# Kernel optimization log

Measured on AMD Instinct MI355X. Metric: run time of the kernel, lower is better.

## Reference

```python
import jax, jax.numpy as jnp
import numpy as np

N, E = 100000, 500000
IN_CH, OUT_CH, MSG_DIM, TIME_DIM, HEADS = 128, 128, 128, 128, 2
C = OUT_CH // HEADS  # per-head channels
EDGE_DIM = MSG_DIM + TIME_DIM


def setup_inputs() -> dict:
    key = jax.random.key(0)
    ks = jax.random.split(key, 16)
    inp = {
        "x": jax.random.normal(ks[0], (N, IN_CH), jnp.float32),
        "last_update": jax.random.uniform(ks[1], (N,), jnp.float32) * 1000.0,
        "t": jax.random.uniform(ks[2], (E,), jnp.float32) * 1000.0,
        "msg": jax.random.normal(ks[3], (E, MSG_DIM), jnp.float32),
        "edge_index": jax.random.randint(ks[4], (2, E), 0, N, jnp.int64),
        # TimeEncoder: Linear(1, TIME_DIM) then cos
        "time_w": jax.random.normal(ks[5], (TIME_DIM,), jnp.float32) / jnp.sqrt(1.0),
        "time_b": jax.random.normal(ks[6], (TIME_DIM,), jnp.float32) * 0.02,
        # TransformerConv linears (stored [in, out] for x @ W)
        "Wq": jax.random.normal(ks[7], (IN_CH, HEADS * C), jnp.float32) / np.sqrt(IN_CH),
        "bq": jnp.zeros((HEADS * C,), jnp.float32),
        "Wk": jax.random.normal(ks[8], (IN_CH, HEADS * C), jnp.float32) / np.sqrt(IN_CH),
        "bk": jnp.zeros((HEADS * C,), jnp.float32),
        "Wv": jax.random.normal(ks[9], (IN_CH, HEADS * C), jnp.float32) / np.sqrt(IN_CH),
        "bv": jnp.zeros((HEADS * C,), jnp.float32),
        "We": jax.random.normal(ks[10], (EDGE_DIM, HEADS * C), jnp.float32) / np.sqrt(EDGE_DIM),  # lin_edge, no bias
        "Wskip": jax.random.normal(ks[11], (IN_CH, HEADS * C), jnp.float32) / np.sqrt(IN_CH),
        "bskip": jnp.zeros((HEADS * C,), jnp.float32),
    }
    return inp


def reference(x, last_update, t, msg, edge_index, time_w, time_b,
              Wq, bq, Wk, bk, Wv, bv, We, Wskip, bskip):
    src = edge_index[0]
    dst = edge_index[1]

    # relative time encoding: cos(Linear(1 -> TIME_DIM))
    rel_t = t - last_update[src]                              # [E]
    rel_t_enc = jnp.cos(rel_t[:, None] * time_w[None, :] + time_b[None, :])  # [E, T]
    edge_attr = jnp.concatenate([rel_t_enc, msg], axis=-1)    # [E, EDGE_DIM]

    # project nodes, then gather per-edge (query at dst, key/value at src)
    q = (x @ Wq + bq).reshape(N, HEADS, C)[dst]               # [E, H, C]
    k = (x @ Wk + bk).reshape(N, HEADS, C)[src]
    v = (x @ Wv + bv).reshape(N, HEADS, C)[src]
    e = (edge_attr @ We).reshape(E, HEADS, C)                 # [E, H, C]

    k = k + e
    alpha = jnp.sum(q * k, axis=-1) / jnp.sqrt(jnp.float32(C))  # [E, H]

    # segment softmax over edges sharing the same destination node
    m = jax.ops.segment_max(alpha, dst, num_segments=N)       # [N, H]
    alpha = jnp.exp(alpha - m[dst])
    s = jax.ops.segment_sum(alpha, dst, num_segments=N)       # [N, H]
    alpha = alpha / (s[dst] + 1e-16)

    # weighted value (value also receives edge projection), scatter-add to dst
    out_e = (v + e) * alpha[..., None]                        # [E, H, C]
    out = jax.ops.segment_sum(out_e, dst, num_segments=N)     # [N, H, C]
    out = out.reshape(N, HEADS * C)

    # root/skip connection
    out = out + x @ Wskip + bskip
    return out
```

## Files before the change

### kernel.cpp

```cpp
#include <hip/hip_runtime.h>
#include <hip/hip_bf16.h>

#define NN 100000
#define EE 500000

typedef __attribute__((ext_vector_type(8))) short short8v;
typedef __attribute__((ext_vector_type(4))) float f32x4;

__device__ __forceinline__ short f2bf(float f) {
  unsigned u = __builtin_bit_cast(unsigned, f);
  u += 0x7fffu + ((u >> 16) & 1u);
  return (short)(u >> 16);
}

__device__ __forceinline__ void barlds() {
  asm volatile("s_waitcnt lgkmcnt(0)" ::: "memory");
  __builtin_amdgcn_s_barrier();
  asm volatile("" ::: "memory");
}

__global__ __launch_bounds__(256) void k_prep(
    const float* __restrict__ Wq, const float* __restrict__ Wk,
    const float* __restrict__ Wv, const float* __restrict__ Wsk,
    const float* __restrict__ We,
    short* __restrict__ Btfrag, short* __restrict__ Wefrag)
{
  int idx = blockIdx.x * 256 + threadIdx.x;
  if (idx < 65536) {
    int b = idx & 7, lane = (idx >> 3) & 63, kt = (idx >> 9) & 3, tn = (idx >> 11) & 7, cb = idx >> 14;
    int k = kt * 32 + (lane >> 4) * 8 + b;
    int c = tn * 16 + (lane & 15);
    const float* W = cb == 0 ? Wq : cb == 1 ? Wk : cb == 2 ? Wv : Wsk;
    Btfrag[idx] = f2bf(W[k * 128 + c]);
  } else if (idx < 98304) {
    int i2 = idx - 65536;
    int b = i2 & 7, lane = (i2 >> 3) & 63, kt = (i2 >> 9) & 7, strip = i2 >> 12;
    int k = kt * 32 + (lane >> 4) * 8 + b;
    int c = strip * 16 + (lane & 15);
    Wefrag[i2] = f2bf(We[k * 128 + c]);
  }
}

__global__ __launch_bounds__(256) void k_xcast(const float* __restrict__ x,
                                               unsigned short* __restrict__ xb)
{
  size_t base = ((size_t)blockIdx.x * 256 + threadIdx.x) * 8;
  f32x4 a = *(const f32x4*)(x + base);
  f32x4 b = *(const f32x4*)(x + base + 4);
  short8v w;
  #pragma unroll
  for (int j = 0; j < 4; ++j) { w[j] = f2bf(a[j]); w[4 + j] = f2bf(b[j]); }
  *(short8v*)(xb + base) = w;
}

__global__ __launch_bounds__(256) void k_zero(int* __restrict__ p, int n)
{
  int i = blockIdx.x * 256 + threadIdx.x;
  if (i < n) p[i] = 0;
}

__global__ __launch_bounds__(256) void k_hist(const int* __restrict__ ei, int* __restrict__ cnt)
{
  int e = blockIdx.x * 256 + threadIdx.x;
  if (e < EE) atomicAdd(&cnt[ei[EE + e]], 1);
}

__global__ __launch_bounds__(256) void k_scan_a(const int* __restrict__ cnt,
    int* __restrict__ offtmp, int* __restrict__ bsum)
{
  __shared__ int sc[256];
  int t = threadIdx.x;
  int i = blockIdx.x * 256 + t;
  int v = (i < NN) ? cnt[i] : 0;
  sc[t] = v;
  __syncthreads();
  for (int d = 1; d < 256; d <<= 1) {
    int add = (t >= d) ? sc[t - d] : 0;
    __syncthreads();
    sc[t] += add;
    __syncthreads();
  }
  if (i < NN) offtmp[i] = sc[t] - v;
  if (t == 255) bsum[blockIdx.x] = sc[255];
}

__global__ __launch_bounds__(512) void k_scan_b(const int* __restrict__ bsum,
                                                int* __restrict__ bbase)
{
  __shared__ int sc[512];
  int t = threadIdx.x;
  int v = (t < 391) ? bsum[t] : 0;
  sc[t] = v;
  __syncthreads();
  for (int d = 1; d < 512; d <<= 1) {
    int add = (t >= d) ? sc[t - d] : 0;
    __syncthreads();
    sc[t] += add;
    __syncthreads();
  }
  bbase[t] = sc[t] - v;
}

__global__ __launch_bounds__(256) void k_scatter(const int* __restrict__ ei,
    const float* __restrict__ tt, const float* __restrict__ lu,
    const int* __restrict__ offtmp, const int* __restrict__ bbase,
    int* __restrict__ cur, int4* __restrict__ emeta)
{
  int e = blockIdx.x * 256 + threadIdx.x;
  if (e < EE) {
    int d = ei[EE + e];
    int pos = offtmp[d] + bbase[d >> 8] + atomicAdd(&cur[d], 1);
    int sv = ei[e];
    int4 m;
    m.x = e; m.y = sv; m.z = d;
    m.w = __float_as_int(tt[e] - lu[sv]);
    emeta[pos] = m;
  }
}

template<int USE_MP>
__global__ __launch_bounds__(512) void k_main(
    const unsigned short* __restrict__ xb, const float* __restrict__ msg,
    const unsigned short* __restrict__ msgb,
    const float* __restrict__ tw, const float* __restrict__ tb,
    const short* __restrict__ Btfrag, const short* __restrict__ Wefrag,
    const float* __restrict__ bq, const float* __restrict__ bk,
    const float* __restrict__ bv, const float* __restrict__ bsk,
    const int* __restrict__ offtmp, const int* __restrict__ bbase,
    const int4* __restrict__ emeta, float* __restrict__ out)
{
  __shared__ short R[24576];
  __shared__ short QL[64 * 128];
  __shared__ float sdenL[128];
  __shared__ int dslot[64];

  short* const XS = R;
  short* const EAT = R + 8192;
  short* const KL = R;
  short* const VT = R + 8192;
  short* const PLm = R + 16384;
  short* const PLm2 = R + 20480;

  const int tid = threadIdx.x;
  const int nb0 = blockIdx.x * 64;
  const int wid = tid >> 6, lane = tid & 63;
  const int g = lane >> 4, lr = lane & 15, l7 = lr & 7;
  const int el = tid >> 3, p = tid & 7;
  const int er7 = el & 7;
  const int psw = p ^ er7;
  const int cme = wid * 16 + lr;
  const int cmeh = cme >> 3, cml = cme & 7;

  const float bqc = bq[cme], bkc = bk[cme], bvc = bv[cme], bskc = bsk[cme];
  const short8v ONEB = {16256,16256,16256,16256,16256,16256,16256,16256};

  {
    int node = nb0 + el;
    short8v a = {0,0,0,0,0,0,0,0}, b = a;
    if (node < NN) {
      const unsigned short* xp = xb + (size_t)node * 128 + p * 8;
      a = *(const short8v*)xp;
      b = *(const short8v*)(xp + 64);
    }
    *(short8v*)&XS[el * 128 + psw * 8] = a;
    *(short8v*)&XS[el * 128 + psw * 8 + 64] = b;
  }
  barlds();
  f32x4 skp[4];
  {
    f32x4 qacc[4];
    #pragma unroll
    for (int eg = 0; eg < 4; ++eg) {
      qacc[eg] = (f32x4){0.f, 0.f, 0.f, 0.f};
      skp[eg] = qacc[eg];
    }
    #pragma unroll
    for (int kt = 0; kt < 4; ++kt) {
      short8v bqf = *(const short8v*)(Btfrag + (size_t)(((0 + wid) * 4 + kt) * 64 + lane) * 8);
      short8v bsf = *(const short8v*)(Btfrag + (size_t)(((24 + wid) * 4 + kt) * 64 + lane) * 8);
      const int sw = (((kt << 2) | g) ^ l7) << 3;
      #pragma unroll
      for (int eg = 0; eg < 4; ++eg) {
        const short8v a = *(const short8v*)&XS[(eg * 16 + lr) * 128 + sw];
        qacc[eg] = __builtin_amdgcn_mfma_f32_16x16x32_bf16(a, bqf, qacc[eg], 0, 0, 0);
        skp[eg] = __builtin_amdgcn_mfma_f32_16x16x32_bf16(a, bsf, skp[eg], 0, 0, 0);
      }
    }
    #pragma unroll
    for (int eg = 0; eg < 4; ++eg)
      #pragma unroll
      for (int rg = 0; rg < 4; ++rg) {
        int row = eg * 16 + g * 4 + rg;
        QL[row * 128 + ((cmeh ^ (row & 7)) << 3) + cml] = f2bf(qacc[eg][rg] + bqc);
      }
  }

  const int beg = offtmp[nb0] + bbase[nb0 >> 8];
  const int end = (nb0 + 64 < NN) ? (offtmp[nb0 + 64] + bbase[(nb0 + 64) >> 8]) : EE;

  f32x4 acc[4], sdacc;
  #pragma unroll
  for (int rtt = 0; rtt < 4; ++rtt) acc[rtt] = (f32x4){0.f, 0.f, 0.f, 0.f};
  sdacc = (f32x4){0.f, 0.f, 0.f, 0.f};

  int pdst = 0; float prelt = 0.f; bool pval = false;
  short8v px0 = {0,0,0,0,0,0,0,0}, px1 = px0, pmb0 = px0, pmb1 = px0;
  {
    int i = beg + el;
    pval = i < end;
    if (pval) {
      int4 m = emeta[i];
      pdst = m.z; prelt = __int_as_float(m.w);
      const unsigned short* xp = xb + (size_t)m.y * 128 + p * 8;
      px0 = *(const short8v*)xp;
      px1 = *(const short8v*)(xp + 64);
      if constexpr (USE_MP) {
        const unsigned short* mp = msgb + (size_t)m.x * 128 + p * 8;
        pmb0 = *(const short8v*)mp;
        pmb1 = *(const short8v*)(mp + 64);
      } else {
        const float* mp = msg + (size_t)m.x * 128 + p * 8;
        f32x4 m0 = *(const f32x4*)mp,        m1 = *(const f32x4*)(mp + 4);
        f32x4 m2 = *(const f32x4*)(mp + 64), m3 = *(const f32x4*)(mp + 68);
        #pragma unroll
        for (int j = 0; j < 4; ++j) {
          pmb0[j] = f2bf(m0[j]); pmb0[4 + j] = f2bf(m1[j]);
          pmb1[j] = f2bf(m2[j]); pmb1[4 + j] = f2bf(m3[j]);
        }
      }
    }
  }
  barlds();

  for (int t0 = beg; t0 < end; t0 += 64) {
    if (p == 0) dslot[el] = pval ? (pdst - nb0) : -1;
    *(short8v*)&XS[el * 128 + psw * 8] = px0;
    *(short8v*)&XS[el * 128 + psw * 8 + 64] = px1;
    *(short8v*)&EAT[el * 256 + 128 + psw * 8] = pmb0;
    *(short8v*)&EAT[el * 256 + 128 + psw * 8 + 64] = pmb1;
    {
      f32x4 w0 = *(const f32x4*)(tw + p * 8),      w1 = *(const f32x4*)(tw + p * 8 + 4);
      f32x4 b0 = *(const f32x4*)(tb + p * 8),      b1 = *(const f32x4*)(tb + p * 8 + 4);
      f32x4 w2 = *(const f32x4*)(tw + p * 8 + 64), w3 = *(const f32x4*)(tw + p * 8 + 68);
      f32x4 b2 = *(const f32x4*)(tb + p * 8 + 64), b3 = *(const f32x4*)(tb + p * 8 + 68);
      short8v ta, tb2;
      #pragma unroll
      for (int j = 0; j < 4; ++j) {
        ta[j]      = f2bf(__cosf(fmaf(prelt, w0[j], b0[j])));
        ta[4 + j]  = f2bf(__cosf(fmaf(prelt, w1[j], b1[j])));
        tb2[j]     = f2bf(__cosf(fmaf(prelt, w2[j], b2[j])));
        tb2[4 + j] = f2bf(__cosf(fmaf(prelt, w3[j], b3[j])));
      }
      *(short8v*)&EAT[el * 256 + psw * 8] = ta;
      *(short8v*)&EAT[el * 256 + psw * 8 + 64] = tb2;
    }
    barlds();

    {
      int i = t0 + 64 + el;
      pval = i < end;
      if (pval) {
        int4 m = emeta[i];
        pdst = m.z; prelt = __int_as_float(m.w);
        const unsigned short* xp = xb + (size_t)m.y * 128 + p * 8;
        px0 = *(const short8v*)xp;
        px1 = *(const short8v*)(xp + 64);
        if constexpr (USE_MP) {
          const unsigned short* mp = msgb + (size_t)m.x * 128 + p * 8;
          pmb0 = *(const short8v*)mp;
          pmb1 = *(const short8v*)(mp + 64);
        } else {
          const float* mp = msg + (size_t)m.x * 128 + p * 8;
          f32x4 m0 = *(const f32x4*)mp,        m1 = *(const f32x4*)(mp + 4);
          f32x4 m2 = *(const f32x4*)(mp + 64), m3 = *(const f32x4*)(mp + 68);
          #pragma unroll
          for (int j = 0; j < 4; ++j) {
            pmb0[j] = f2bf(m0[j]); pmb0[4 + j] = f2bf(m1[j]);
            pmb1[j] = f2bf(m2[j]); pmb1[4 + j] = f2bf(m3[j]);
          }
        }
      }
    }

    f32x4 ae[4];
    ae[0] = (f32x4){0.f, 0.f, 0.f, 0.f}; ae[1] = ae[0]; ae[2] = ae[0]; ae[3] = ae[0];
    #pragma unroll
    for (int kt = 0; kt < 8; ++kt) {
      short8v wef = *(const short8v*)(Wefrag + (size_t)((wid * 8 + kt) * 64 + lane) * 8);
      const int sw = (((kt << 2) | g) ^ l7) << 3;
      #pragma unroll
      for (int eg = 0; eg < 4; ++eg) {
        const short8v a = *(const short8v*)&EAT[(eg * 16 + lr) * 256 + sw];
        ae[eg] = __builtin_amdgcn_mfma_f32_16x16x32_bf16(a, wef, ae[eg], 0, 0, 0);
      }
    }
    f32x4 ak[4], av[4];
    ak[0] = (f32x4){0.f, 0.f, 0.f, 0.f}; ak[1] = ak[0]; ak[2] = ak[0]; ak[3] = ak[0];
    av[0] = ak[0]; av[1] = ak[0]; av[2] = ak[0]; av[3] = ak[0];
    #pragma unroll
    for (int kt = 0; kt < 4; ++kt) {
      short8v wkf = *(const short8v*)(Btfrag + (size_t)(((8 + wid) * 4 + kt) * 64 + lane) * 8);
      short8v wvf = *(const short8v*)(Btfrag + (size_t)(((16 + wid) * 4 + kt) * 64 + lane) * 8);
      const int sw = (((kt << 2) | g) ^ l7) << 3;
      #pragma unroll
      for (int eg = 0; eg < 4; ++eg) {
        const short8v a = *(const short8v*)&XS[(eg * 16 + lr) * 128 + sw];
        ak[eg] = __builtin_amdgcn_mfma_f32_16x16x32_bf16(a, wkf, ak[eg], 0, 0, 0);
        av[eg] = __builtin_amdgcn_mfma_f32_16x16x32_bf16(a, wvf, av[eg], 0, 0, 0);
      }
    }
    barlds();

    #pragma unroll
    for (int eg = 0; eg < 4; ++eg)
      #pragma unroll
      for (int rg = 0; rg < 4; ++rg) {
        int e = eg * 16 + g * 4 + rg;
        float kh = ak[eg][rg] + bkc + ae[eg][rg];
        float vh = av[eg][rg] + bvc + ae[eg][rg];
        KL[e * 128 + ((cmeh ^ (e & 7)) << 3) + cml] = f2bf(kh);
        VT[cme * 64 + ((((e >> 3) ^ cml)) << 3) + (e & 7)] = f2bf(vh);
      }
    barlds();

    {
      const int rt = wid >> 1, ct0 = (wid & 1) * 2;
      short8v qa[4];
      #pragma unroll
      for (int kt = 0; kt < 4; ++kt)
        qa[kt] = *(const short8v*)&QL[(rt * 16 + lr) * 128 + ((((kt << 2) | g) ^ l7) << 3)];
      #pragma unroll
      for (int c2 = 0; c2 < 2; ++c2) {
        const int ct = ct0 + c2;
        f32x4 s0 = (f32x4){0.f, 0.f, 0.f, 0.f};
        f32x4 s1 = (f32x4){0.f, 0.f, 0.f, 0.f};
        #pragma unroll
        for (int kt = 0; kt < 4; ++kt) {
          const short8v kbf = *(const short8v*)&KL[(ct * 16 + lr) * 128 + ((((kt << 2) | g) ^ l7) << 3)];
          if (kt < 2) s0 = __builtin_amdgcn_mfma_f32_16x16x32_bf16(qa[kt], kbf, s0, 0, 0, 0);
          else        s1 = __builtin_amdgcn_mfma_f32_16x16x32_bf16(qa[kt], kbf, s1, 0, 0, 0);
        }
        const int col = ct * 16 + lr;
        const int dsc = dslot[col];
        #pragma unroll
        for (int rg = 0; rg < 4; ++rg) {
          int row = rt * 16 + g * 4 + rg;
          bool hit = (dsc == row);
          float pv0 = hit ? __expf(s0[rg] * 0.125f) : 0.f;
          float pv1 = hit ? __expf(s1[rg] * 0.125f) : 0.f;
          int off = row * 64 + ((((col >> 3) ^ (row & 7))) << 3) + (col & 7);
          PLm[off] = f2bf(pv0);
          PLm2[off] = f2bf(pv1);
        }
      }
    }
    barlds();

    {
      const short* PH = (wid < 4) ? PLm : PLm2;
      const int rt4 = wid & 3;
      const short8v vb0 = *(const short8v*)&VT[cme * 64 + ((g ^ cml) << 3)];
      const short8v vb1 = *(const short8v*)&VT[cme * 64 + (((4 | g) ^ cml) << 3)];
      #pragma unroll
      for (int rtt = 0; rtt < 4; ++rtt) {
        const short8v pa0 = *(const short8v*)&PH[(rtt * 16 + lr) * 64 + ((g ^ l7) << 3)];
        const short8v pa1 = *(const short8v*)&PH[(rtt * 16 + lr) * 64 + (((4 | g) ^ l7) << 3)];
        acc[rtt] = __builtin_amdgcn_mfma_f32_16x16x32_bf16(pa0, vb0, acc[rtt], 0, 0, 0);
        acc[rtt] = __builtin_amdgcn_mfma_f32_16x16x32_bf16(pa1, vb1, acc[rtt], 0, 0, 0);
        if (rt4 == rtt) {
          sdacc = __builtin_amdgcn_mfma_f32_16x16x32_bf16(pa0, ONEB, sdacc, 0, 0, 0);
          sdacc = __builtin_amdgcn_mfma_f32_16x16x32_bf16(pa1, ONEB, sdacc, 0, 0, 0);
        }
      }
    }
    barlds();
  }

  if (lr == 0) {
    #pragma unroll
    for (int rg = 0; rg < 4; ++rg)
      sdenL[(wid >> 2) * 64 + (wid & 3) * 16 + g * 4 + rg] = sdacc[rg];
  }
  barlds();
  #pragma unroll
  for (int rtt = 0; rtt < 4; ++rtt)
    #pragma unroll
    for (int rg = 0; rg < 4; ++rg) {
      int row = rtt * 16 + g * 4 + rg;
      int node = nb0 + row;
      if (node < NN) {
        float den = sdenL[(wid >> 2) * 64 + row] + 1e-16f;
        out[(size_t)node * 128 + cme] = skp[rtt][rg] + bskc + acc[rtt][rg] / den;
      }
    }
}

extern "C" void kernel_launch(void* const* d_in, const int* in_sizes, int n_in,
                              void* d_out, int out_size, void* d_ws, size_t ws_size,
                              hipStream_t stream) {
  const float* x    = (const float*)d_in[0];
  const float* lu   = (const float*)d_in[1];
  const float* tt   = (const float*)d_in[2];
  const float* msg  = (const float*)d_in[3];
  const int*   ei   = (const int*)d_in[4];
  const float* timew = (const float*)d_in[5];
  const float* timeb = (const float*)d_in[6];
  const float* Wq   = (const float*)d_in[7];
  const float* bq   = (const float*)d_in[8];
  const float* Wk   = (const float*)d_in[9];
  const float* bk   = (const float*)d_in[10];
  const float* Wv   = (const float*)d_in[11];
  const float* bv   = (const float*)d_in[12];
  const float* We   = (const float*)d_in[13];
  const float* Wsk  = (const float*)d_in[14];
  const float* bsk  = (const float*)d_in[15];
  float* out = (float*)d_out;

  char* wsp = (char*)d_ws;
  unsigned short* xbw  = (unsigned short*)wsp;
  short* Btfrag = (short*)(wsp + 51200000);
  short* Wefrag = (short*)(wsp + 51331072);
  int* cnt      = (int*)(wsp + 51404800);
  int* cur      = (int*)(wsp + 51804800);
  int* offtmp   = (int*)(wsp + 52204800);
  int* bsum     = (int*)(wsp + 52605184);
  int* bbase    = (int*)(wsp + 52607232);
  int4* emeta   = (int4*)(wsp + 54609280);
  unsigned short* msgb = (unsigned short*)(wsp + 62609280);
  const int use_mp = (ws_size >= (size_t)190609280) ? 1 : 0;

  k_zero<<<782, 256, 0, stream>>>(cnt, 200000);
  k_prep<<<384, 256, 0, stream>>>(Wq, Wk, Wv, Wsk, We, Btfrag, Wefrag);
  k_xcast<<<6250, 256, 0, stream>>>(x, xbw);
  if (use_mp) k_xcast<<<31250, 256, 0, stream>>>(msg, msgb);
  k_hist<<<1954, 256, 0, stream>>>(ei, cnt);
  k_scan_a<<<391, 256, 0, stream>>>(cnt, offtmp, bsum);
  k_scan_b<<<1, 512, 0, stream>>>(bsum, bbase);
  k_scatter<<<1954, 256, 0, stream>>>(ei, tt, lu, offtmp, bbase, cur, emeta);
  if (use_mp) {
    k_main<1><<<1563, 512, 0, stream>>>(xbw, msg, msgb, timew, timeb,
                                        Btfrag, Wefrag, bq, bk, bv, bsk,
                                        offtmp, bbase, emeta, out);
  } else {
    k_main<0><<<1563, 512, 0, stream>>>(xbw, msg, msgb, timew, timeb,
                                        Btfrag, Wefrag, bq, bk, bv, bsk,
                                        offtmp, bbase, emeta, out);
  }
}
```

Measured before the change: 418.4 us.

## Unalias LDS buffers to drop barriers, pad strides, and drop msg bf16 precast

Gives the main kernel separate padded LDS buffers for x, msg, time encoding, Q, K, V and P instead of one aliased region. With no aliasing, the barrier between the K/V projection and the K/V stores, and the barrier at the end of each edge-tile iteration, can both be removed. The separate msg pre-cast kernel and its bf16 buffer are also removed, so the main kernel always reads fp32 msg and converts it inline. This trades a large increase in LDS per block, which likely cuts blocks per CU, and more global bytes read in the main kernel, for fewer barriers and one less full pass over msg.

```diff
diff --git a/kernel.cpp b/kernel.cpp
--- a/kernel.cpp
+++ b/kernel.cpp
@@ -118,10 +118,8 @@
   }
 }
 
-template<int USE_MP>
 __global__ __launch_bounds__(512) void k_main(
     const unsigned short* __restrict__ xb, const float* __restrict__ msg,
-    const unsigned short* __restrict__ msgb,
     const float* __restrict__ tw, const float* __restrict__ tb,
     const short* __restrict__ Btfrag, const short* __restrict__ Wefrag,
     const float* __restrict__ bq, const float* __restrict__ bk,
@@ -129,17 +127,16 @@
     const int* __restrict__ offtmp, const int* __restrict__ bbase,
     const int4* __restrict__ emeta, float* __restrict__ out)
 {
-  __shared__ short R[24576];
-  __shared__ short QL[64 * 128];
+  __shared__ short XS[64 * 136];
+  __shared__ short MS[64 * 136];
+  __shared__ short TEs[64 * 136];
+  __shared__ short QL[64 * 136];
+  __shared__ short KL[64 * 136];
+  __shared__ short VT[128 * 72];
+  __shared__ short PLm[64 * 72];
+  __shared__ short PLm2[64 * 72];
   __shared__ float sdenL[128];
   __shared__ int dslot[64];
-
-  short* const XS = R;
-  short* const EAT = R + 8192;
-  short* const KL = R;
-  short* const VT = R + 8192;
-  short* const PLm = R + 16384;
-  short* const PLm2 = R + 20480;
 
   const int tid = threadIdx.x;
   const int nb0 = blockIdx.x * 64;
@@ -162,8 +159,8 @@
       a = *(const short8v*)xp;
       b = *(const short8v*)(xp + 64);
     }
-    *(short8v*)&XS[el * 128 + psw * 8] = a;
-    *(short8v*)&XS[el * 128 + psw * 8 + 64] = b;
+    *(short8v*)&XS[el * 136 + psw * 8] = a;
+    *(short8v*)&XS[el * 136 + psw * 8 + 64] = b;
   }
   barlds();
   f32x4 skp[4];
@@ -181,7 +178,7 @@
       const int sw = (((kt << 2) | g) ^ l7) << 3;
       #pragma unroll
       for (int eg = 0; eg < 4; ++eg) {
-        const short8v a = *(const short8v*)&XS[(eg * 16 + lr) * 128 + sw];
+        const short8v a = *(const short8v*)&XS[(eg * 16 + lr) * 136 + sw];
         qacc[eg] = __builtin_amdgcn_mfma_f32_16x16x32_bf16(a, bqf, qacc[eg], 0, 0, 0);
         skp[eg] = __builtin_amdgcn_mfma_f32_16x16x32_bf16(a, bsf, skp[eg], 0, 0, 0);
       }
@@ -191,7 +188,7 @@
       #pragma unroll
       for (int rg = 0; rg < 4; ++rg) {
         int row = eg * 16 + g * 4 + rg;
-        QL[row * 128 + ((cmeh ^ (row & 7)) << 3) + cml] = f2bf(qacc[eg][rg] + bqc);
+        QL[row * 136 + ((cmeh ^ (row & 7)) << 3) + cml] = f2bf(qacc[eg][rg] + bqc);
       }
   }
 
@@ -214,19 +211,13 @@
       const unsigned short* xp = xb + (size_t)m.y * 128 + p * 8;
       px0 = *(const short8v*)xp;
       px1 = *(const short8v*)(xp + 64);
-      if constexpr (USE_MP) {
-        const unsigned short* mp = msgb + (size_t)m.x * 128 + p * 8;
-        pmb0 = *(const short8v*)mp;
-        pmb1 = *(const short8v*)(mp + 64);
-      } else {
-        const float* mp = msg + (size_t)m.x * 128 + p * 8;
-        f32x4 m0 = *(const f32x4*)mp,        m1 = *(const f32x4*)(mp + 4);
-        f32x4 m2 = *(const f32x4*)(mp + 64), m3 = *(const f32x4*)(mp + 68);
-        #pragma unroll
-        for (int j = 0; j < 4; ++j) {
-          pmb0[j] = f2bf(m0[j]); pmb0[4 + j] = f2bf(m1[j]);
-          pmb1[j] = f2bf(m2[j]); pmb1[4 + j] = f2bf(m3[j]);
-        }
+      const float* mp = msg + (size_t)m.x * 128 + p * 8;
+      f32x4 m0 = *(const f32x4*)mp,        m1 = *(const f32x4*)(mp + 4);
+      f32x4 m2 = *(const f32x4*)(mp + 64), m3 = *(const f32x4*)(mp + 68);
+      #pragma unroll
+      for (int j = 0; j < 4; ++j) {
+        pmb0[j] = f2bf(m0[j]); pmb0[4 + j] = f2bf(m1[j]);
+        pmb1[j] = f2bf(m2[j]); pmb1[4 + j] = f2bf(m3[j]);
       }
     }
   }
@@ -234,10 +225,10 @@
 
   for (int t0 = beg; t0 < end; t0 += 64) {
     if (p == 0) dslot[el] = pval ? (pdst - nb0) : -1;
-    *(short8v*)&XS[el * 128 + psw * 8] = px0;
-    *(short8v*)&XS[el * 128 + psw * 8 + 64] = px1;
-    *(short8v*)&EAT[el * 256 + 128 + psw * 8] = pmb0;
-    *(short8v*)&EAT[el * 256 + 128 + psw * 8 + 64] = pmb1;
+    *(short8v*)&XS[el * 136 + psw * 8] = px0;
+    *(short8v*)&XS[el * 136 + psw * 8 + 64] = px1;
+    *(short8v*)&MS[el * 136 + psw * 8] = pmb0;
+    *(short8v*)&MS[el * 136 + psw * 8 + 64] = pmb1;
     {
       f32x4 w0 = *(const f32x4*)(tw + p * 8),      w1 = *(const f32x4*)(tw + p * 8 + 4);
       f32x4 b0 = *(const f32x4*)(tb + p * 8),      b1 = *(const f32x4*)(tb + p * 8 + 4);
@@ -251,8 +242,8 @@
         tb2[j]     = f2bf(__cosf(fmaf(prelt, w2[j], b2[j])));
         tb2[4 + j] = f2bf(__cosf(fmaf(prelt, w3[j], b3[j])));
       }
-      *(short8v*)&EAT[el * 256 + psw * 8] = ta;
-      *(short8v*)&EAT[el * 256 + psw * 8 + 64] = tb2;
+      *(short8v*)&TEs[el * 136 + psw * 8] = ta;
+      *(short8v*)&TEs[el * 136 + psw * 8 + 64] = tb2;
     }
     barlds();
 
@@ -265,19 +256,13 @@
         const unsigned short* xp = xb + (size_t)m.y * 128 + p * 8;
         px0 = *(const short8v*)xp;
         px1 = *(const short8v*)(xp + 64);
-        if constexpr (USE_MP) {
-          const unsigned short* mp = msgb + (size_t)m.x * 128 + p * 8;
-          pmb0 = *(const short8v*)mp;
-          pmb1 = *(const short8v*)(mp + 64);
-        } else {
-          const float* mp = msg + (size_t)m.x * 128 + p * 8;
-          f32x4 m0 = *(const f32x4*)mp,        m1 = *(const f32x4*)(mp + 4);
-          f32x4 m2 = *(const f32x4*)(mp + 64), m3 = *(const f32x4*)(mp + 68);
-          #pragma unroll
-          for (int j = 0; j < 4; ++j) {
-            pmb0[j] = f2bf(m0[j]); pmb0[4 + j] = f2bf(m1[j]);
-            pmb1[j] = f2bf(m2[j]); pmb1[4 + j] = f2bf(m3[j]);
-          }
+        const float* mp = msg + (size_t)m.x * 128 + p * 8;
+        f32x4 m0 = *(const f32x4*)mp,        m1 = *(const f32x4*)(mp + 4);
+        f32x4 m2 = *(const f32x4*)(mp + 64), m3 = *(const f32x4*)(mp + 68);
+        #pragma unroll
+        for (int j = 0; j < 4; ++j) {
+          pmb0[j] = f2bf(m0[j]); pmb0[4 + j] = f2bf(m1[j]);
+          pmb1[j] = f2bf(m2[j]); pmb1[4 + j] = f2bf(m3[j]);
         }
       }
     }
@@ -285,12 +270,22 @@
     f32x4 ae[4];
     ae[0] = (f32x4){0.f, 0.f, 0.f, 0.f}; ae[1] = ae[0]; ae[2] = ae[0]; ae[3] = ae[0];
     #pragma unroll
-    for (int kt = 0; kt < 8; ++kt) {
+    for (int kt = 0; kt < 4; ++kt) {
       short8v wef = *(const short8v*)(Wefrag + (size_t)((wid * 8 + kt) * 64 + lane) * 8);
       const int sw = (((kt << 2) | g) ^ l7) << 3;
       #pragma unroll
       for (int eg = 0; eg < 4; ++eg) {
-        const short8v a = *(const short8v*)&EAT[(eg * 16 + lr) * 256 + sw];
+        const short8v a = *(const short8v*)&TEs[(eg * 16 + lr) * 136 + sw];
+        ae[eg] = __builtin_amdgcn_mfma_f32_16x16x32_bf16(a, wef, ae[eg], 0, 0, 0);
+      }
+    }
+    #pragma unroll
+    for (int kt = 0; kt < 4; ++kt) {
+      short8v wef = *(const short8v*)(Wefrag + (size_t)((wid * 8 + kt + 4) * 64 + lane) * 8);
+      const int sw = (((kt << 2) | g) ^ l7) << 3;
+      #pragma unroll
+      for (int eg = 0; eg < 4; ++eg) {
+        const short8v a = *(const short8v*)&MS[(eg * 16 + lr) * 136 + sw];
         ae[eg] = __builtin_amdgcn_mfma_f32_16x16x32_bf16(a, wef, ae[eg], 0, 0, 0);
       }
     }
@@ -304,13 +299,11 @@
       const int sw = (((kt << 2) | g) ^ l7) << 3;
       #pragma unroll
       for (int eg = 0; eg < 4; ++eg) {
-        const short8v a = *(const short8v*)&XS[(eg * 16 + lr) * 128 + sw];
+        const short8v a = *(const short8v*)&XS[(eg * 16 + lr) * 136 + sw];
         ak[eg] = __builtin_amdgcn_mfma_f32_16x16x32_bf16(a, wkf, ak[eg], 0, 0, 0);
         av[eg] = __builtin_amdgcn_mfma_f32_16x16x32_bf16(a, wvf, av[eg], 0, 0, 0);
       }
     }
-    barlds();
-
     #pragma unroll
     for (int eg = 0; eg < 4; ++eg)
       #pragma unroll
@@ -318,8 +311,8 @@
         int e = eg * 16 + g * 4 + rg;
         float kh = ak[eg][rg] + bkc + ae[eg][rg];
         float vh = av[eg][rg] + bvc + ae[eg][rg];
-        KL[e * 128 + ((cmeh ^ (e & 7)) << 3) + cml] = f2bf(kh);
-        VT[cme * 64 + ((((e >> 3) ^ cml)) << 3) + (e & 7)] = f2bf(vh);
+        KL[e * 136 + ((cmeh ^ (e & 7)) << 3) + cml] = f2bf(kh);
+        VT[cme * 72 + ((((e >> 3) ^ cml)) << 3) + (e & 7)] = f2bf(vh);
       }
     barlds();
 
@@ -328,7 +321,7 @@
       short8v qa[4];
       #pragma unroll
       for (int kt = 0; kt < 4; ++kt)
-        qa[kt] = *(const short8v*)&QL[(rt * 16 + lr) * 128 + ((((kt << 2) | g) ^ l7) << 3)];
+        qa[kt] = *(const short8v*)&QL[(rt * 16 + lr) * 136 + ((((kt << 2) | g) ^ l7) << 3)];
       #pragma unroll
       for (int c2 = 0; c2 < 2; ++c2) {
         const int ct = ct0 + c2;
@@ -336,7 +329,7 @@
         f32x4 s1 = (f32x4){0.f, 0.f, 0.f, 0.f};
         #pragma unroll
         for (int kt = 0; kt < 4; ++kt) {
-          const short8v kbf = *(const short8v*)&KL[(ct * 16 + lr) * 128 + ((((kt << 2) | g) ^ l7) << 3)];
+          const short8v kbf = *(const short8v*)&KL[(ct * 16 + lr) * 136 + ((((kt << 2) | g) ^ l7) << 3)];
           if (kt < 2) s0 = __builtin_amdgcn_mfma_f32_16x16x32_bf16(qa[kt], kbf, s0, 0, 0, 0);
           else        s1 = __builtin_amdgcn_mfma_f32_16x16x32_bf16(qa[kt], kbf, s1, 0, 0, 0);
         }
@@ -348,7 +341,7 @@
           bool hit = (dsc == row);
           float pv0 = hit ? __expf(s0[rg] * 0.125f) : 0.f;
           float pv1 = hit ? __expf(s1[rg] * 0.125f) : 0.f;
-          int off = row * 64 + ((((col >> 3) ^ (row & 7))) << 3) + (col & 7);
+          int off = row * 72 + ((((col >> 3) ^ (row & 7))) << 3) + (col & 7);
           PLm[off] = f2bf(pv0);
           PLm2[off] = f2bf(pv1);
         }
@@ -359,12 +352,12 @@
     {
       const short* PH = (wid < 4) ? PLm : PLm2;
       const int rt4 = wid & 3;
-      const short8v vb0 = *(const short8v*)&VT[cme * 64 + ((g ^ cml) << 3)];
-      const short8v vb1 = *(const short8v*)&VT[cme * 64 + (((4 | g) ^ cml) << 3)];
+      const short8v vb0 = *(const short8v*)&VT[cme * 72 + ((g ^ cml) << 3)];
+      const short8v vb1 = *(const short8v*)&VT[cme * 72 + (((4 | g) ^ cml) << 3)];
       #pragma unroll
       for (int rtt = 0; rtt < 4; ++rtt) {
-        const short8v pa0 = *(const short8v*)&PH[(rtt * 16 + lr) * 64 + ((g ^ l7) << 3)];
-        const short8v pa1 = *(const short8v*)&PH[(rtt * 16 + lr) * 64 + (((4 | g) ^ l7) << 3)];
+        const short8v pa0 = *(const short8v*)&PH[(rtt * 16 + lr) * 72 + ((g ^ l7) << 3)];
+        const short8v pa1 = *(const short8v*)&PH[(rtt * 16 + lr) * 72 + (((4 | g) ^ l7) << 3)];
         acc[rtt] = __builtin_amdgcn_mfma_f32_16x16x32_bf16(pa0, vb0, acc[rtt], 0, 0, 0);
         acc[rtt] = __builtin_amdgcn_mfma_f32_16x16x32_bf16(pa1, vb1, acc[rtt], 0, 0, 0);
         if (rt4 == rtt) {
@@ -373,9 +366,9 @@
         }
       }
     }
-    barlds();
-  }
-
+  }
+
+  barlds();
   if (lr == 0) {
     #pragma unroll
     for (int rg = 0; rg < 4; ++rg)
@@ -426,24 +419,15 @@
   int* bsum     = (int*)(wsp + 52605184);
   int* bbase    = (int*)(wsp + 52607232);
   int4* emeta   = (int4*)(wsp + 54609280);
-  unsigned short* msgb = (unsigned short*)(wsp + 62609280);
-  const int use_mp = (ws_size >= (size_t)190609280) ? 1 : 0;
 
   k_zero<<<782, 256, 0, stream>>>(cnt, 200000);
   k_prep<<<384, 256, 0, stream>>>(Wq, Wk, Wv, Wsk, We, Btfrag, Wefrag);
   k_xcast<<<6250, 256, 0, stream>>>(x, xbw);
-  if (use_mp) k_xcast<<<31250, 256, 0, stream>>>(msg, msgb);
   k_hist<<<1954, 256, 0, stream>>>(ei, cnt);
   k_scan_a<<<391, 256, 0, stream>>>(cnt, offtmp, bsum);
   k_scan_b<<<1, 512, 0, stream>>>(bsum, bbase);
   k_scatter<<<1954, 256, 0, stream>>>(ei, tt, lu, offtmp, bbase, cur, emeta);
-  if (use_mp) {
-    k_main<1><<<1563, 512, 0, stream>>>(xbw, msg, msgb, timew, timeb,
-                                        Btfrag, Wefrag, bq, bk, bv, bsk,
-                                        offtmp, bbase, emeta, out);
-  } else {
-    k_main<0><<<1563, 512, 0, stream>>>(xbw, msg, msgb, timew, timeb,
-                                        Btfrag, Wefrag, bq, bk, bv, bsk,
-                                        offtmp, bbase, emeta, out);
-  }
-}
+  k_main<<<1563, 512, 0, stream>>>(xbw, msg, timew, timeb,
+                                   Btfrag, Wefrag, bq, bk, bv, bsk,
+                                   offtmp, bbase, emeta, out);
+}
```

Result: slower. 436.8 us (+4.4%).

## Give each LDS tile its own buffer and drop two per-iteration barriers

Applied to the files above, without the earlier changes.

Replaces the aliased shared-memory region with separate XS, MS, time-encoding, KL, VT and P buffers. Because the tiles no longer overlap, the barrier between the projection MFMAs and the K/V stores can be removed, along with the barrier at the end of each edge-tile iteration. The edge projection is split into two K-loops, one over the time-encoding tile and one over the message tile. This roughly doubles LDS use per 512-thread block, which likely limits the CU to one resident block instead of two. It also risks a race where dslot is rewritten at the top of the next iteration while other waves are still reading it.

```diff
diff --git a/kernel.cpp b/kernel.cpp
--- a/kernel.cpp
+++ b/kernel.cpp
@@ -129,17 +129,16 @@
     const int* __restrict__ offtmp, const int* __restrict__ bbase,
     const int4* __restrict__ emeta, float* __restrict__ out)
 {
-  __shared__ short R[24576];
+  __shared__ short XS[64 * 128];
+  __shared__ short MS[64 * 128];
+  __shared__ short TEs[64 * 128];
   __shared__ short QL[64 * 128];
+  __shared__ short KL[64 * 128];
+  __shared__ short VT[128 * 64];
+  __shared__ short PLm[64 * 64];
+  __shared__ short PLm2[64 * 64];
   __shared__ float sdenL[128];
   __shared__ int dslot[64];
-
-  short* const XS = R;
-  short* const EAT = R + 8192;
-  short* const KL = R;
-  short* const VT = R + 8192;
-  short* const PLm = R + 16384;
-  short* const PLm2 = R + 20480;
 
   const int tid = threadIdx.x;
   const int nb0 = blockIdx.x * 64;
@@ -236,8 +235,8 @@
     if (p == 0) dslot[el] = pval ? (pdst - nb0) : -1;
     *(short8v*)&XS[el * 128 + psw * 8] = px0;
     *(short8v*)&XS[el * 128 + psw * 8 + 64] = px1;
-    *(short8v*)&EAT[el * 256 + 128 + psw * 8] = pmb0;
-    *(short8v*)&EAT[el * 256 + 128 + psw * 8 + 64] = pmb1;
+    *(short8v*)&MS[el * 128 + psw * 8] = pmb0;
+    *(short8v*)&MS[el * 128 + psw * 8 + 64] = pmb1;
     {
       f32x4 w0 = *(const f32x4*)(tw + p * 8),      w1 = *(const f32x4*)(tw + p * 8 + 4);
       f32x4 b0 = *(const f32x4*)(tb + p * 8),      b1 = *(const f32x4*)(tb + p * 8 + 4);
@@ -251,8 +250,8 @@
         tb2[j]     = f2bf(__cosf(fmaf(prelt, w2[j], b2[j])));
         tb2[4 + j] = f2bf(__cosf(fmaf(prelt, w3[j], b3[j])));
       }
-      *(short8v*)&EAT[el * 256 + psw * 8] = ta;
-      *(short8v*)&EAT[el * 256 + psw * 8 + 64] = tb2;
+      *(short8v*)&TEs[el * 128 + psw * 8] = ta;
+      *(short8v*)&TEs[el * 128 + psw * 8 + 64] = tb2;
     }
     barlds();
 
@@ -285,12 +284,22 @@
     f32x4 ae[4];
     ae[0] = (f32x4){0.f, 0.f, 0.f, 0.f}; ae[1] = ae[0]; ae[2] = ae[0]; ae[3] = ae[0];
     #pragma unroll
-    for (int kt = 0; kt < 8; ++kt) {
+    for (int kt = 0; kt < 4; ++kt) {
       short8v wef = *(const short8v*)(Wefrag + (size_t)((wid * 8 + kt) * 64 + lane) * 8);
       const int sw = (((kt << 2) | g) ^ l7) << 3;
       #pragma unroll
       for (int eg = 0; eg < 4; ++eg) {
-        const short8v a = *(const short8v*)&EAT[(eg * 16 + lr) * 256 + sw];
+        const short8v a = *(const short8v*)&TEs[(eg * 16 + lr) * 128 + sw];
+        ae[eg] = __builtin_amdgcn_mfma_f32_16x16x32_bf16(a, wef, ae[eg], 0, 0, 0);
+      }
+    }
+    #pragma unroll
+    for (int kt = 0; kt < 4; ++kt) {
+      short8v wef = *(const short8v*)(Wefrag + (size_t)((wid * 8 + kt + 4) * 64 + lane) * 8);
+      const int sw = (((kt << 2) | g) ^ l7) << 3;
+      #pragma unroll
+      for (int eg = 0; eg < 4; ++eg) {
+        const short8v a = *(const short8v*)&MS[(eg * 16 + lr) * 128 + sw];
         ae[eg] = __builtin_amdgcn_mfma_f32_16x16x32_bf16(a, wef, ae[eg], 0, 0, 0);
       }
     }
@@ -309,8 +318,6 @@
         av[eg] = __builtin_amdgcn_mfma_f32_16x16x32_bf16(a, wvf, av[eg], 0, 0, 0);
       }
     }
-    barlds();
-
     #pragma unroll
     for (int eg = 0; eg < 4; ++eg)
       #pragma unroll
@@ -373,9 +380,9 @@
         }
       }
     }
-    barlds();
-  }
-
+  }
+
+  barlds();
   if (lr == 0) {
     #pragma unroll
     for (int rg = 0; rg < 4; ++rg)
```

Result: no change. 420.5 us (+0.5%).
